# Optimization experiments

Hardware: AMD Instinct MI355X
Metric: run time of the kernel (lower is better)

## Reference

```python
import jax, jax.numpy as jnp
import numpy as np

A_CUBIC = -0.75  # torch grid_sample bicubic convolution coefficient
INTERP_FACTOR = 0.25
WINDOW = 20
STEP = 4


def _cubic_interp_1d(signal):
    # Replicates torch bicubic grid_sample (align_corners=True, border padding)
    # on a (B,1,1,n) tensor, which reduces to 1D cubic convolution (A=-0.75).
    B, n = signal.shape
    num_points = int((n - 1) / INTERP_FACTOR) + 1
    pos = jnp.linspace(0.0, n - 1, num_points)  # sample positions in index space
    i0 = jnp.floor(pos).astype(jnp.int32)
    s = (pos - i0).astype(signal.dtype)  # frac in [0,1)
    A = A_CUBIC
    def w_far(d):   # 1 <= d <= 2
        return ((A * d - 5 * A) * d + 8 * A) * d - 4 * A
    def w_near(d):  # 0 <= d <= 1
        return ((A + 2) * d - (A + 3)) * d * d + 1
    w = jnp.stack([w_far(s + 1), w_near(s), w_near(1 - s), w_far(2 - s)], axis=-1)  # (P,4)
    idx = jnp.clip(i0[:, None] + jnp.arange(-1, 3)[None, :], 0, n - 1)  # border pad, (P,4)
    vals = signal[:, idx]  # (B,P,4)
    return jnp.einsum('bpk,pk->bp', vals, w)


def _apply_kernels(x, gamma_raw):
    # per-row shift so min >= 0 (only if min < 0), then softmax-weighted kernel mix
    m = jnp.min(x, axis=1, keepdims=True)
    x = x - jnp.minimum(m, 0.0)
    gamma = jax.nn.softmax(gamma_raw)
    poly = (x + 1.3) ** 2                      # polynomial: degree=2, offset=1.3
    gauss = jnp.exp(-0.5 * (x - 0.7) ** 2)     # gaussian: center=0.7, sigma=1.0
    return gamma[0] * poly + gamma[1] * gauss


def setup_inputs() -> dict:
    key = jax.random.key(0)
    return {
        'signal': jax.random.normal(key, (4, 1000), dtype=jnp.float32),
        'alpha': jnp.float32(0.15),
        'beta': jnp.float32(0.9),
        'gamma_raw': jnp.array([0.5, 0.5], dtype=jnp.float32),
    }


def reference(signal, alpha, beta, gamma_raw):
    interp = _cubic_interp_1d(signal)              # (B, n)
    ks = _apply_kernels(interp, gamma_raw)         # (B, n)
    B, n = ks.shape
    n_windows = (n - WINDOW) // STEP + 1
    starts = jnp.arange(n_windows) * STEP          # (W,)
    posn = jnp.arange(n)                           # (n,)
    in_win = (posn[None, :] >= starts[:, None]) & (posn[None, :] < starts[:, None] + WINDOW)
    in_win = in_win.astype(ks.dtype)               # (W, n)
    sig = ks[:, None, :]                           # (B,1,n)
    # M: fft of zero-padded window; M1: fft of signal with window zeroed out
    M = jnp.abs(jnp.fft.fft(sig * in_win[None], axis=-1))          # (B,W,n)
    M1 = jnp.abs(jnp.fft.fft(sig * (1.0 - in_win)[None], axis=-1))  # (B,W,n)
    x_max = jnp.max(M, axis=-1, keepdims=True)
    strong = (M > x_max * alpha).astype(M.dtype)
    combined = M1 * M * strong
    result = jnp.minimum(M, combined)              # (B,W,n)
    thr = beta * jnp.max(result.reshape(B, -1), axis=1)[:, None, None]
    result = result * (result > thr).astype(result.dtype)
    return result
```

## Files before the change

kernel.cpp:

```cpp
#include <hip/hip_runtime.h>
#include <math.h>

#define NSIG 1000
#define NP   3997
#define KHALF 1999
#define NW   995
#define WIN  20
#define STEPW 4
#define BATCH 4
#define NCH  125
#define CW   8
#define RS   2000


__device__ __forceinline__ double interp_at(const float* __restrict__ s, int p) {
    int i0 = p >> 2;
    int si = p & 3;
    double ss = 0.25 * (double)si;
    const double A = -0.75;
    double d0 = ss + 1.0;
    double w0 = ((A * d0 - 5.0 * A) * d0 + 8.0 * A) * d0 - 4.0 * A;
    double w1 = ((A + 2.0) * ss - (A + 3.0)) * ss * ss + 1.0;
    double d2 = 1.0 - ss;
    double w2 = ((A + 2.0) * d2 - (A + 3.0)) * d2 * d2 + 1.0;
    double d3 = 2.0 - ss;
    double w3 = ((A * d3 - 5.0 * A) * d3 + 8.0 * A) * d3 - 4.0 * A;
    int im1 = i0 - 1; if (im1 < 0) im1 = 0;
    int ip1 = i0 + 1; if (ip1 > NSIG - 1) ip1 = NSIG - 1;
    int ip2 = i0 + 2; if (ip2 > NSIG - 1) ip2 = NSIG - 1;
    return w0 * (double)s[im1] + w1 * (double)s[i0] +
           w2 * (double)s[ip1] + w3 * (double)s[ip2];
}

__global__ __launch_bounds__(256) void init_kernel(
        const float* __restrict__ sig, const float* __restrict__ gamma_raw,
        float* __restrict__ ks, float2* __restrict__ tw,
        unsigned int* __restrict__ rmax) {
    int bx = blockIdx.x;
    int tid = threadIdx.x;
    if (bx < 16) {
        int m = bx * 256 + tid;
        if (m < NP) {
            double ang = -6.283185307179586476925286766559 * ((double)m / (double)NP);
            double sv, cv; sincos(ang, &sv, &cv);
            tw[m] = make_float2((float)cv, (float)sv);
        }
        if (bx == 0 && tid < BATCH) rmax[tid] = 0u;
        return;
    }
    __shared__ double red[256];
    int b = bx - 16;
    const float* srow = sig + b * NSIG;
    double lmin = 1e300;
    for (int p = tid; p < NP; p += 256)
        lmin = fmin(lmin, interp_at(srow, p));
    red[tid] = lmin;
    __syncthreads();
    for (int s = 128; s > 0; s >>= 1) {
        if (tid < s) red[tid] = fmin(red[tid], red[tid + s]);
        __syncthreads();
    }
    double m = fmin(red[0], 0.0);
    double g0r = (double)gamma_raw[0], g1r = (double)gamma_raw[1];
    double mx = fmax(g0r, g1r);
    double e0 = exp(g0r - mx), e1 = exp(g1r - mx);
    double inv = 1.0 / (e0 + e1);
    double g0 = e0 * inv, g1 = e1 * inv;
    for (int p = tid; p < NP; p += 256) {
        double x = interp_at(srow, p) - m;
        double poly = (x + 1.3) * (x + 1.3);
        double gauss = exp(-0.5 * (x - 0.7) * (x - 0.7));
        ks[b * NP + p] = (float)(g0 * poly + g1 * gauss);
    }
}

__global__ __launch_bounds__(256) void dft_kernel(const float* __restrict__ ks,
                                                  float2* __restrict__ S) {
    __shared__ float  lks[NP];
    __shared__ double2 red[256];
    int b = blockIdx.y;
    int tid = threadIdx.x;
    int kk = tid & 7;
    int tc = tid >> 3;
    int k = blockIdx.x * 8 + kk;
    for (int i = tid; i < NP; i += 256) lks[i] = ks[b * NP + i];
    __syncthreads();

    double sr = 0.0, si = 0.0;
    if (k < KHALF) {
        int t0 = tc * 125;
        int t1 = t0 + 125; if (t1 > NP) t1 = NP;
        const double TWO_PI = 6.283185307179586476925286766559;
        double base = -TWO_PI / (double)NP;
        double rr, ri;
        sincos(base * (double)k, &ri, &rr);
        int m0 = (k * t0) % NP;
        double pr, pi;
        sincos(base * (double)m0, &pi, &pr);
        for (int t = t0; t < t1; ++t) {
            double kv = (double)lks[t];
            sr = fma(kv, pr, sr);
            si = fma(kv, pi, si);
            double nr = pr * rr - pi * ri;
            double ni = pr * ri + pi * rr;
            pr = nr; pi = ni;
        }
    }
    red[tid] = make_double2(sr, si);
    __syncthreads();
    for (int s = 128; s >= 8; s >>= 1) {
        if (tid < s) {
            red[tid].x += red[tid + s].x;
            red[tid].y += red[tid + s].y;
        }
        __syncthreads();
    }
    if (tid < 8) {
        int kw = blockIdx.x * 8 + tid;
        if (kw < KHALF)
            S[b * NP + kw] = make_float2((float)red[tid].x, (float)red[tid].y);
    }
}

__device__ __forceinline__ float wavemax(float x) {
    #pragma unroll
    for (int off = 32; off > 0; off >>= 1)
        x = fmaxf(x, __shfl_xor(x, off));
    return x;
}

#define SLIDE1(n, co, cn) { \
    float ax = fmaf((cn), T##n.x, -(co)); \
    float ay = (cn) * T##n.y; \
    Wx##n = fmaf(ax, Q##n.x, fmaf(-ay, Q##n.y, Wx##n)); \
    Wy##n = fmaf(ax, Q##n.y, fmaf(ay, Q##n.x, Wy##n)); \
    float tq = fmaf(Q##n.x, R##n.x, -(Q##n.y * R##n.y)); \
    Q##n.y = fmaf(Q##n.x, R##n.y, Q##n.y * R##n.x); \
    Q##n.x = tq; }

#define SLIDEJ(co, cn) SLIDE1(0, co, cn) SLIDE1(1, co, cn) SLIDE1(2, co, cn) SLIDE1(3, co, cn)

#define SLIDE4(base) { \
    { float co = kp[(base) + 0], cn = kp[(base) + 20]; SLIDEJ(co, cn) } \
    { float co = kp[(base) + 1], cn = kp[(base) + 21]; SLIDEJ(co, cn) } \
    { float co = kp[(base) + 2], cn = kp[(base) + 22]; SLIDEJ(co, cn) } \
    { float co = kp[(base) + 3], cn = kp[(base) + 23]; SLIDEJ(co, cn) } }

#define WINBODY(w) { \
    float M0 = sqrtf(fmaf(Wx0, Wx0, Wy0 * Wy0)); \
    float M1m = sqrtf(fmaf(Wx1, Wx1, Wy1 * Wy1)); \
    float M2m = sqrtf(fmaf(Wx2, Wx2, Wy2 * Wy2)); \
    float M3m = sqrtf(fmaf(Wx3, Wx3, Wy3 * Wy3)); \
    float lm = fmaxf(fmaxf(M0, M1m), fmaxf(M2m, v3 ? M3m : 0.f)); \
    lm = wavemax(lm); \
    if ((tid & 63) == 0) wred[tid >> 6] = lm; \
    __syncthreads(); \
    float bm = fmaxf(fmaxf(fmaxf(wred[0], wred[1]), fmaxf(wred[2], wred[3])), \
                     fmaxf(fmaxf(wred[4], wred[5]), fmaxf(wred[6], wred[7]))); \
    float cut = bm * alpha; \
    __syncthreads(); \
    if (w0 + (w) < NW) { \
        float r0v = 0.f, r1v = 0.f, r2v = 0.f, r3v = 0.f; \
        { float dr = Sv0.x - Wx0, di = Sv0.y - Wy0; float m1 = sqrtf(fmaf(dr, dr, di * di)); \
          if (M0 > cut) r0v = fminf(M0, m1 * M0); } \
        { float dr = Sv1.x - Wx1, di = Sv1.y - Wy1; float m1 = sqrtf(fmaf(dr, dr, di * di)); \
          if (M1m > cut) r1v = fminf(M1m, m1 * M1m); } \
        { float dr = Sv2.x - Wx2, di = Sv2.y - Wy2; float m1 = sqrtf(fmaf(dr, dr, di * di)); \
          if (M2m > cut) r2v = fminf(M2m, m1 * M2m); } \
        { float dr = Sv3.x - Wx3, di = Sv3.y - Wy3; float m1 = sqrtf(fmaf(dr, dr, di * di)); \
          if (M3m > cut) r3v = fminf(M3m, m1 * M3m); } \
        float* rp = resc + rbase + (size_t)(w) * RS; \
        rp[k0] = r0v; rp[k1] = r1v; rp[k2] = r2v; if (v3) rp[k3] = r3v; \
        rl = fmaxf(rl, fmaxf(fmaxf(r0v, r1v), fmaxf(r2v, r3v))); \
    } }

__global__ __launch_bounds__(512, 4) void window_kernel(
        const float* __restrict__ ks, const float2* __restrict__ tw,
        const float2* __restrict__ S, const float* __restrict__ alpha_p,
        float* __restrict__ resc, float* __restrict__ cmax,
        unsigned int* __restrict__ rmax) {
    __shared__ float wred[8];
    int b = blockIdx.y;
    int wc = blockIdx.x;
    int w0 = wc * CW;
    int s0 = w0 * STEPW;
    int tid = threadIdx.x;
    float alpha = *alpha_p;
    const float* kp = ks + b * NP + s0;

    int k0 = tid, k1 = tid + 512, k2 = tid + 1024, k3 = tid + 1536;
    bool v3 = (k3 < KHALF);

    float2 R0 = tw[k0], R1 = tw[k1], R2 = tw[k2], R3 = tw[k3];
    float2 T0 = tw[(20 * k0) % NP], T1 = tw[(20 * k1) % NP],
           T2 = tw[(20 * k2) % NP], T3 = tw[(20 * k3) % NP];
    float2 Q0 = tw[(k0 * s0) % NP], Q1 = tw[(k1 * s0) % NP],
           Q2 = tw[(k2 * s0) % NP], Q3 = tw[(k3 * s0) % NP];
    const float2* Sb = S + b * NP;
    float2 Sv0 = Sb[k0], Sv1 = Sb[k1], Sv2 = Sb[k2], Sv3 = Sb[k3];

    float Dx0 = kp[19], Dy0 = 0.f, Dx1 = kp[19], Dy1 = 0.f,
          Dx2 = kp[19], Dy2 = 0.f, Dx3 = kp[19], Dy3 = 0.f;
    #pragma unroll
    for (int j = 18; j >= 0; --j) {
        float a = kp[j];
        float nx, ny;
        nx = fmaf(Dx0, R0.x, fmaf(-Dy0, R0.y, a));
        ny = fmaf(Dy0, R0.x, Dx0 * R0.y);
        Dx0 = nx; Dy0 = ny;
        nx = fmaf(Dx1, R1.x, fmaf(-Dy1, R1.y, a));
        ny = fmaf(Dy1, R1.x, Dx1 * R1.y);
        Dx1 = nx; Dy1 = ny;
        nx = fmaf(Dx2, R2.x, fmaf(-Dy2, R2.y, a));
        ny = fmaf(Dy2, R2.x, Dx2 * R2.y);
        Dx2 = nx; Dy2 = ny;
        nx = fmaf(Dx3, R3.x, fmaf(-Dy3, R3.y, a));
        ny = fmaf(Dy3, R3.x, Dx3 * R3.y);
        Dx3 = nx; Dy3 = ny;
    }
    float Wx0 = fmaf(Q0.x, Dx0, -(Q0.y * Dy0));
    float Wy0 = fmaf(Q0.x, Dy0, Q0.y * Dx0);
    float Wx1 = fmaf(Q1.x, Dx1, -(Q1.y * Dy1));
    float Wy1 = fmaf(Q1.x, Dy1, Q1.y * Dx1);
    float Wx2 = fmaf(Q2.x, Dx2, -(Q2.y * Dy2));
    float Wy2 = fmaf(Q2.x, Dy2, Q2.y * Dx2);
    float Wx3 = fmaf(Q3.x, Dx3, -(Q3.y * Dy3));
    float Wy3 = fmaf(Q3.x, Dy3, Q3.y * Dx3);

    float rl = 0.f;
    size_t rbase = (size_t)(b * NW + w0) * RS;

    WINBODY(0)
    SLIDE4(0)  WINBODY(1)
    SLIDE4(4)  WINBODY(2)
    SLIDE4(8)  WINBODY(3)
    SLIDE4(12) WINBODY(4)
    SLIDE4(16) WINBODY(5)
    SLIDE4(20) WINBODY(6)
    SLIDE4(24) WINBODY(7)

    rl = wavemax(rl);
    if ((tid & 63) == 0) wred[tid >> 6] = rl;
    __syncthreads();
    if (tid == 0) {
        float bm = fmaxf(fmaxf(fmaxf(wred[0], wred[1]), fmaxf(wred[2], wred[3])),
                         fmaxf(fmaxf(wred[4], wred[5]), fmaxf(wred[6], wred[7])));
        cmax[b * NCH + wc] = bm;
        atomicMax(&rmax[b], __float_as_uint(bm));
    }
}

__global__ __launch_bounds__(1024) void finalize_kernel(
        const float* __restrict__ resc, const float* __restrict__ cmax,
        const unsigned int* __restrict__ rmax, const float* __restrict__ beta_p,
        float* __restrict__ out) {
    int b = blockIdx.y, w = blockIdx.x;
    float thr = (*beta_p) * __uint_as_float(rmax[b]);
    size_t base = (size_t)(b * NW + w) * NP;
    int tid = threadIdx.x;
    if (cmax[b * NCH + (w >> 3)] <= thr) {
        #pragma unroll
        for (int c = 0; c < 4; ++c) {
            int i = tid + c * 1024;
            if (i < NP) out[base + i] = 0.f;
        }
        return;
    }
    const float* rp = resc + (size_t)(b * NW + w) * RS;
    #pragma unroll
    for (int c = 0; c < 2; ++c) {
        int k = tid + c * 1024;
        if (k < KHALF) {
            float v = rp[k];
            float f = (v > thr) ? v : 0.f;
            out[base + k] = f;
            if (k > 0) out[base + NP - k] = f;
        }
    }
}

extern "C" void kernel_launch(void* const* d_in, const int* in_sizes, int n_in,
                              void* d_out, int out_size, void* d_ws, size_t ws_size,
                              hipStream_t stream) {
    const float* sig       = (const float*)d_in[0];
    const float* alpha_p   = (const float*)d_in[1];
    const float* beta_p    = (const float*)d_in[2];
    const float* gamma_raw = (const float*)d_in[3];
    char* ws = (char*)d_ws;
    float*        ks   = (float*)(ws + 0);
    float2*       tw   = (float2*)(ws + 65536);
    float2*       S    = (float2*)(ws + 98304);
    unsigned int* rmax = (unsigned int*)(ws + 226304);
    float*        cmax = (float*)(ws + 226432);
    float*        resc = (float*)(ws + 262144);
    float* out = (float*)d_out;

    hipLaunchKernelGGL(init_kernel,     dim3(20),         dim3(256),  0, stream, sig, gamma_raw, ks, tw, rmax);
    hipLaunchKernelGGL(dft_kernel,      dim3(250, BATCH), dim3(256),  0, stream, ks, S);
    hipLaunchKernelGGL(window_kernel,   dim3(NCH, BATCH), dim3(512),  0, stream, ks, tw, S, alpha_p, resc, cmax, rmax);
    hipLaunchKernelGGL(finalize_kernel, dim3(NW, BATCH),  dim3(1024), 0, stream, resc, cmax, rmax, beta_p, out);
}
```

Before: 70.29 us.

## Fuse all stages into one cooperative persistent kernel with grid syncs

Measured after the change: 269.5 us. 283% more time.

```diff
diff --git a/kernel.cpp b/kernel.cpp
--- a/kernel.cpp
+++ b/kernel.cpp
@@ -1,5 +1,8 @@
 #include <hip/hip_runtime.h>
+#include <hip/hip_cooperative_groups.h>
 #include <math.h>
+
+namespace cg = cooperative_groups;
 
 #define NSIG 1000
 #define NP   3997
@@ -11,6 +14,8 @@
 #define NCH  125
 #define CW   8
 #define RS   2000
+#define NBLK 256
+#define NTASK (NCH * BATCH)
 
 
 __device__ __forceinline__ double interp_at(const float* __restrict__ s, int p) {
@@ -30,96 +35,6 @@
     int ip2 = i0 + 2; if (ip2 > NSIG - 1) ip2 = NSIG - 1;
     return w0 * (double)s[im1] + w1 * (double)s[i0] +
            w2 * (double)s[ip1] + w3 * (double)s[ip2];
-}
-
-__global__ __launch_bounds__(256) void init_kernel(
-        const float* __restrict__ sig, const float* __restrict__ gamma_raw,
-        float* __restrict__ ks, float2* __restrict__ tw,
-        unsigned int* __restrict__ rmax) {
-    int bx = blockIdx.x;
-    int tid = threadIdx.x;
-    if (bx < 16) {
-        int m = bx * 256 + tid;
-        if (m < NP) {
-            double ang = -6.283185307179586476925286766559 * ((double)m / (double)NP);
-            double sv, cv; sincos(ang, &sv, &cv);
-            tw[m] = make_float2((float)cv, (float)sv);
-        }
-        if (bx == 0 && tid < BATCH) rmax[tid] = 0u;
-        return;
-    }
-    __shared__ double red[256];
-    int b = bx - 16;
-    const float* srow = sig + b * NSIG;
-    double lmin = 1e300;
-    for (int p = tid; p < NP; p += 256)
-        lmin = fmin(lmin, interp_at(srow, p));
-    red[tid] = lmin;
-    __syncthreads();
-    for (int s = 128; s > 0; s >>= 1) {
-        if (tid < s) red[tid] = fmin(red[tid], red[tid + s]);
-        __syncthreads();
-    }
-    double m = fmin(red[0], 0.0);
-    double g0r = (double)gamma_raw[0], g1r = (double)gamma_raw[1];
-    double mx = fmax(g0r, g1r);
-    double e0 = exp(g0r - mx), e1 = exp(g1r - mx);
-    double inv = 1.0 / (e0 + e1);
-    double g0 = e0 * inv, g1 = e1 * inv;
-    for (int p = tid; p < NP; p += 256) {
-        double x = interp_at(srow, p) - m;
-        double poly = (x + 1.3) * (x + 1.3);
-        double gauss = exp(-0.5 * (x - 0.7) * (x - 0.7));
-        ks[b * NP + p] = (float)(g0 * poly + g1 * gauss);
-    }
-}
-
-__global__ __launch_bounds__(256) void dft_kernel(const float* __restrict__ ks,
-                                                  float2* __restrict__ S) {
-    __shared__ float  lks[NP];
-    __shared__ double2 red[256];
-    int b = blockIdx.y;
-    int tid = threadIdx.x;
-    int kk = tid & 7;
-    int tc = tid >> 3;
-    int k = blockIdx.x * 8 + kk;
-    for (int i = tid; i < NP; i += 256) lks[i] = ks[b * NP + i];
-    __syncthreads();
-
-    double sr = 0.0, si = 0.0;
-    if (k < KHALF) {
-        int t0 = tc * 125;
-        int t1 = t0 + 125; if (t1 > NP) t1 = NP;
-        const double TWO_PI = 6.283185307179586476925286766559;
-        double base = -TWO_PI / (double)NP;
-        double rr, ri;
-        sincos(base * (double)k, &ri, &rr);
-        int m0 = (k * t0) % NP;
-        double pr, pi;
-        sincos(base * (double)m0, &pi, &pr);
-        for (int t = t0; t < t1; ++t) {
-            double kv = (double)lks[t];
-            sr = fma(kv, pr, sr);
-            si = fma(kv, pi, si);
-            double nr = pr * rr - pi * ri;
-            double ni = pr * ri + pi * rr;
-            pr = nr; pi = ni;
-        }
-    }
-    red[tid] = make_double2(sr, si);
-    __syncthreads();
-    for (int s = 128; s >= 8; s >>= 1) {
-        if (tid < s) {
-            red[tid].x += red[tid + s].x;
-            red[tid].y += red[tid + s].y;
-        }
-        __syncthreads();
-    }
-    if (tid < 8) {
-        int kw = blockIdx.x * 8 + tid;
-        if (kw < KHALF)
-            S[b * NP + kw] = make_float2((float)red[tid].x, (float)red[tid].y);
-    }
 }
 
 __device__ __forceinline__ float wavemax(float x) {
@@ -174,107 +89,200 @@
         rl = fmaxf(rl, fmaxf(fmaxf(r0v, r1v), fmaxf(r2v, r3v))); \
     } }
 
-__global__ __launch_bounds__(512, 4) void window_kernel(
-        const float* __restrict__ ks, const float2* __restrict__ tw,
-        const float2* __restrict__ S, const float* __restrict__ alpha_p,
-        float* __restrict__ resc, float* __restrict__ cmax,
-        unsigned int* __restrict__ rmax) {
-    __shared__ float wred[8];
-    int b = blockIdx.y;
-    int wc = blockIdx.x;
-    int w0 = wc * CW;
-    int s0 = w0 * STEPW;
+__global__ __launch_bounds__(512, 2) void mega_kernel(
+        const float* __restrict__ sig, const float* __restrict__ alpha_p,
+        const float* __restrict__ beta_p, const float* __restrict__ gamma_raw,
+        float* __restrict__ ks, float2* __restrict__ tw, float2* __restrict__ S,
+        unsigned int* __restrict__ rmax, float* __restrict__ cmax,
+        float* __restrict__ resc, float* __restrict__ out) {
+    cg::grid_group grid = cg::this_grid();
+    int bid = blockIdx.x;
     int tid = threadIdx.x;
+
+    __shared__ float   lks[NP];
+    __shared__ double2 redd[512];
+    __shared__ float   wred[8];
+
+    if (bid < 8) {
+        int m = bid * 512 + tid;
+        if (m < NP) {
+            double ang = -6.283185307179586476925286766559 * ((double)m / (double)NP);
+            double sv, cv; sincos(ang, &sv, &cv);
+            tw[m] = make_float2((float)cv, (float)sv);
+        }
+        if (bid == 0 && tid < BATCH) rmax[tid] = 0u;
+    } else if (bid < 8 + BATCH) {
+        int b = bid - 8;
+        const float* srow = sig + b * NSIG;
+        double lmin = 1e300;
+        for (int p = tid; p < NP; p += 512)
+            lmin = fmin(lmin, interp_at(srow, p));
+        redd[tid].x = lmin;
+        __syncthreads();
+        for (int s = 256; s > 0; s >>= 1) {
+            if (tid < s) redd[tid].x = fmin(redd[tid].x, redd[tid + s].x);
+            __syncthreads();
+        }
+        double mm = fmin(redd[0].x, 0.0);
+        double g0r = (double)gamma_raw[0], g1r = (double)gamma_raw[1];
+        double mx = fmax(g0r, g1r);
+        double e0 = exp(g0r - mx), e1 = exp(g1r - mx);
+        double inv = 1.0 / (e0 + e1);
+        double g0 = e0 * inv, g1 = e1 * inv;
+        for (int p = tid; p < NP; p += 512) {
+            double x = interp_at(srow, p) - mm;
+            double poly = (x + 1.3) * (x + 1.3);
+            double gauss = exp(-0.5 * (x - 0.7) * (x - 0.7));
+            ks[b * NP + p] = (float)(g0 * poly + g1 * gauss);
+        }
+    }
+    __threadfence();
+    grid.sync();
+
+    for (int tsk = bid; tsk < NTASK; tsk += NBLK) {
+        int b = tsk & 3, kg = tsk >> 2;
+        __syncthreads();
+        for (int i = tid; i < NP; i += 512) lks[i] = ks[b * NP + i];
+        __syncthreads();
+        int kk = tid & 15, tc = tid >> 4;
+        int k = kg * 16 + kk;
+        double sr = 0.0, si = 0.0;
+        if (k < KHALF) {
+            int t0 = tc * 125;
+            int t1 = t0 + 125; if (t1 > NP) t1 = NP;
+            const double TWO_PI = 6.283185307179586476925286766559;
+            double base = -TWO_PI / (double)NP;
+            double rr, ri;
+            sincos(base * (double)k, &ri, &rr);
+            int m0 = (k * t0) % NP;
+            double pr, pi;
+            sincos(base * (double)m0, &pi, &pr);
+            for (int t = t0; t < t1; ++t) {
+                double kv = (double)lks[t];
+                sr = fma(kv, pr, sr);
+                si = fma(kv, pi, si);
+                double nr = pr * rr - pi * ri;
+                double ni = pr * ri + pi * rr;
+                pr = nr; pi = ni;
+            }
+        }
+        redd[tid] = make_double2(sr, si);
+        __syncthreads();
+        for (int s = 256; s >= 16; s >>= 1) {
+            if (tid < s) {
+                redd[tid].x += redd[tid + s].x;
+                redd[tid].y += redd[tid + s].y;
+            }
+            __syncthreads();
+        }
+        if (tid < 16) {
+            int kw = kg * 16 + tid;
+            if (kw < KHALF)
+                S[b * NP + kw] = make_float2((float)redd[tid].x, (float)redd[tid].y);
+        }
+    }
+    __threadfence();
+    grid.sync();
+
     float alpha = *alpha_p;
-    const float* kp = ks + b * NP + s0;
-
-    int k0 = tid, k1 = tid + 512, k2 = tid + 1024, k3 = tid + 1536;
-    bool v3 = (k3 < KHALF);
-
-    float2 R0 = tw[k0], R1 = tw[k1], R2 = tw[k2], R3 = tw[k3];
-    float2 T0 = tw[(20 * k0) % NP], T1 = tw[(20 * k1) % NP],
-           T2 = tw[(20 * k2) % NP], T3 = tw[(20 * k3) % NP];
-    float2 Q0 = tw[(k0 * s0) % NP], Q1 = tw[(k1 * s0) % NP],
-           Q2 = tw[(k2 * s0) % NP], Q3 = tw[(k3 * s0) % NP];
-    const float2* Sb = S + b * NP;
-    float2 Sv0 = Sb[k0], Sv1 = Sb[k1], Sv2 = Sb[k2], Sv3 = Sb[k3];
-
-    float Dx0 = kp[19], Dy0 = 0.f, Dx1 = kp[19], Dy1 = 0.f,
-          Dx2 = kp[19], Dy2 = 0.f, Dx3 = kp[19], Dy3 = 0.f;
-    #pragma unroll
-    for (int j = 18; j >= 0; --j) {
-        float a = kp[j];
-        float nx, ny;
-        nx = fmaf(Dx0, R0.x, fmaf(-Dy0, R0.y, a));
-        ny = fmaf(Dy0, R0.x, Dx0 * R0.y);
-        Dx0 = nx; Dy0 = ny;
-        nx = fmaf(Dx1, R1.x, fmaf(-Dy1, R1.y, a));
-        ny = fmaf(Dy1, R1.x, Dx1 * R1.y);
-        Dx1 = nx; Dy1 = ny;
-        nx = fmaf(Dx2, R2.x, fmaf(-Dy2, R2.y, a));
-        ny = fmaf(Dy2, R2.x, Dx2 * R2.y);
-        Dx2 = nx; Dy2 = ny;
-        nx = fmaf(Dx3, R3.x, fmaf(-Dy3, R3.y, a));
-        ny = fmaf(Dy3, R3.x, Dx3 * R3.y);
-        Dx3 = nx; Dy3 = ny;
+    for (int tsk = bid; tsk < NTASK; tsk += NBLK) {
+        int b = tsk & 3, wc = tsk >> 2;
+        int w0 = wc * CW;
+        int s0 = w0 * STEPW;
+        const float* kp = ks + b * NP + s0;
+
+        int k0 = tid, k1 = tid + 512, k2 = tid + 1024, k3 = tid + 1536;
+        bool v3 = (k3 < KHALF);
+
+        float2 R0 = tw[k0], R1 = tw[k1], R2 = tw[k2], R3 = tw[k3];
+        float2 T0 = tw[(20 * k0) % NP], T1 = tw[(20 * k1) % NP],
+               T2 = tw[(20 * k2) % NP], T3 = tw[(20 * k3) % NP];
+        float2 Q0 = tw[(k0 * s0) % NP], Q1 = tw[(k1 * s0) % NP],
+               Q2 = tw[(k2 * s0) % NP], Q3 = tw[(k3 * s0) % NP];
+        const float2* Sb = S + b * NP;
+        float2 Sv0 = Sb[k0], Sv1 = Sb[k1], Sv2 = Sb[k2], Sv3 = Sb[k3];
+
+        float Dx0 = kp[19], Dy0 = 0.f, Dx1 = kp[19], Dy1 = 0.f,
+              Dx2 = kp[19], Dy2 = 0.f, Dx3 = kp[19], Dy3 = 0.f;
+        #pragma unroll
+        for (int j = 18; j >= 0; --j) {
+            float a = kp[j];
+            float nx, ny;
+            nx = fmaf(Dx0, R0.x, fmaf(-Dy0, R0.y, a));
+            ny = fmaf(Dy0, R0.x, Dx0 * R0.y);
+            Dx0 = nx; Dy0 = ny;
+            nx = fmaf(Dx1, R1.x, fmaf(-Dy1, R1.y, a));
+            ny = fmaf(Dy1, R1.x, Dx1 * R1.y);
+            Dx1 = nx; Dy1 = ny;
+            nx = fmaf(Dx2, R2.x, fmaf(-Dy2, R2.y, a));
+            ny = fmaf(Dy2, R2.x, Dx2 * R2.y);
+            Dx2 = nx; Dy2 = ny;
+            nx = fmaf(Dx3, R3.x, fmaf(-Dy3, R3.y, a));
+            ny = fmaf(Dy3, R3.x, Dx3 * R3.y);
+            Dx3 = nx; Dy3 = ny;
+        }
+        float Wx0 = fmaf(Q0.x, Dx0, -(Q0.y * Dy0));
+        float Wy0 = fmaf(Q0.x, Dy0, Q0.y * Dx0);
+        float Wx1 = fmaf(Q1.x, Dx1, -(Q1.y * Dy1));
+        float Wy1 = fmaf(Q1.x, Dy1, Q1.y * Dx1);
+        float Wx2 = fmaf(Q2.x, Dx2, -(Q2.y * Dy2));
+        float Wy2 = fmaf(Q2.x, Dy2, Q2.y * Dx2);
+        float Wx3 = fmaf(Q3.x, Dx3, -(Q3.y * Dy3));
+        float Wy3 = fmaf(Q3.x, Dy3, Q3.y * Dx3);
+
+        float rl = 0.f;
+        size_t rbase = (size_t)(b * NW + w0) * RS;
+
+        WINBODY(0)
+        SLIDE4(0)  WINBODY(1)
+        SLIDE4(4)  WINBODY(2)
+        SLIDE4(8)  WINBODY(3)
+        SLIDE4(12) WINBODY(4)
+        SLIDE4(16) WINBODY(5)
+        SLIDE4(20) WINBODY(6)
+        SLIDE4(24) WINBODY(7)
+
+        rl = wavemax(rl);
+        if ((tid & 63) == 0) wred[tid >> 6] = rl;
+        __syncthreads();
+        if (tid == 0) {
+            float bm = fmaxf(fmaxf(fmaxf(wred[0], wred[1]), fmaxf(wred[2], wred[3])),
+                             fmaxf(fmaxf(wred[4], wred[5]), fmaxf(wred[6], wred[7])));
+            cmax[b * NCH + wc] = bm;
+            atomicMax(&rmax[b], __float_as_uint(bm));
+        }
+        __syncthreads();
     }
-    float Wx0 = fmaf(Q0.x, Dx0, -(Q0.y * Dy0));
-    float Wy0 = fmaf(Q0.x, Dy0, Q0.y * Dx0);
-    float Wx1 = fmaf(Q1.x, Dx1, -(Q1.y * Dy1));
-    float Wy1 = fmaf(Q1.x, Dy1, Q1.y * Dx1);
-    float Wx2 = fmaf(Q2.x, Dx2, -(Q2.y * Dy2));
-    float Wy2 = fmaf(Q2.x, Dy2, Q2.y * Dx2);
-    float Wx3 = fmaf(Q3.x, Dx3, -(Q3.y * Dy3));
-    float Wy3 = fmaf(Q3.x, Dy3, Q3.y * Dx3);
-
-    float rl = 0.f;
-    size_t rbase = (size_t)(b * NW + w0) * RS;
-
-    WINBODY(0)
-    SLIDE4(0)  WINBODY(1)
-    SLIDE4(4)  WINBODY(2)
-    SLIDE4(8)  WINBODY(3)
-    SLIDE4(12) WINBODY(4)
-    SLIDE4(16) WINBODY(5)
-    SLIDE4(20) WINBODY(6)
-    SLIDE4(24) WINBODY(7)
-
-    rl = wavemax(rl);
-    if ((tid & 63) == 0) wred[tid >> 6] = rl;
+    __threadfence();
+    grid.sync();
+
+    if (tid < BATCH)
+        wred[tid] = __uint_as_float(atomicMax(&rmax[tid], 0u));
     __syncthreads();
-    if (tid == 0) {
-        float bm = fmaxf(fmaxf(fmaxf(wred[0], wred[1]), fmaxf(wred[2], wred[3])),
-                         fmaxf(fmaxf(wred[4], wred[5]), fmaxf(wred[6], wred[7])));
-        cmax[b * NCH + wc] = bm;
-        atomicMax(&rmax[b], __float_as_uint(bm));
-    }
-}
-
-__global__ __launch_bounds__(1024) void finalize_kernel(
-        const float* __restrict__ resc, const float* __restrict__ cmax,
-        const unsigned int* __restrict__ rmax, const float* __restrict__ beta_p,
-        float* __restrict__ out) {
-    int b = blockIdx.y, w = blockIdx.x;
-    float thr = (*beta_p) * __uint_as_float(rmax[b]);
-    size_t base = (size_t)(b * NW + w) * NP;
-    int tid = threadIdx.x;
-    if (cmax[b * NCH + (w >> 3)] <= thr) {
-        #pragma unroll
-        for (int c = 0; c < 4; ++c) {
-            int i = tid + c * 1024;
-            if (i < NP) out[base + i] = 0.f;
-        }
-        return;
-    }
-    const float* rp = resc + (size_t)(b * NW + w) * RS;
-    #pragma unroll
-    for (int c = 0; c < 2; ++c) {
-        int k = tid + c * 1024;
-        if (k < KHALF) {
-            float v = rp[k];
-            float f = (v > thr) ? v : 0.f;
-            out[base + k] = f;
-            if (k > 0) out[base + NP - k] = f;
+    float beta = *beta_p;
+    for (int rr = bid; rr < BATCH * NW; rr += NBLK) {
+        int b = rr / NW;
+        int w = rr - b * NW;
+        float thr = beta * wred[b];
+        size_t base = (size_t)rr * NP;
+        if (cmax[b * NCH + (w >> 3)] <= thr) {
+            #pragma unroll
+            for (int c = 0; c < 8; ++c) {
+                int i = tid + c * 512;
+                if (i < NP) out[base + i] = 0.f;
+            }
+        } else {
+            const float* rp = resc + (size_t)rr * RS;
+            #pragma unroll
+            for (int c = 0; c < 4; ++c) {
+                int k = tid + c * 512;
+                if (k < KHALF) {
+                    float v = rp[k];
+                    float f = (v > thr) ? v : 0.f;
+                    out[base + k] = f;
+                    if (k > 0) out[base + NP - k] = f;
+                }
+            }
         }
     }
 }
@@ -293,10 +301,11 @@
     unsigned int* rmax = (unsigned int*)(ws + 226304);
     float*        cmax = (float*)(ws + 226432);
     float*        resc = (float*)(ws + 262144);
-    float* out = (float*)d_out;
-
-    hipLaunchKernelGGL(init_kernel,     dim3(20),         dim3(256),  0, stream, sig, gamma_raw, ks, tw, rmax);
-    hipLaunchKernelGGL(dft_kernel,      dim3(250, BATCH), dim3(256),  0, stream, ks, S);
-    hipLaunchKernelGGL(window_kernel,   dim3(NCH, BATCH), dim3(512),  0, stream, ks, tw, S, alpha_p, resc, cmax, rmax);
-    hipLaunchKernelGGL(finalize_kernel, dim3(NW, BATCH),  dim3(1024), 0, stream, resc, cmax, rmax, beta_p, out);
+    float* outp = (float*)d_out;
+
+    void* args[] = { (void*)&sig, (void*)&alpha_p, (void*)&beta_p, (void*)&gamma_raw,
+                     (void*)&ks, (void*)&tw, (void*)&S, (void*)&rmax,
+                     (void*)&cmax, (void*)&resc, (void*)&outp };
+    hipLaunchCooperativeKernel((const void*)mega_kernel, dim3(NBLK), dim3(512),
+                               args, 0, stream);
 }
```

## Fuse init into DFT kernel and recompute window spectra in finalize

Applied to the files above, without the earlier changes.

Result: faster. 61.65 us (-12.3%).

```diff
diff --git a/kernel.cpp b/kernel.cpp
--- a/kernel.cpp
+++ b/kernel.cpp
@@ -10,7 +10,6 @@
 #define BATCH 4
 #define NCH  125
 #define CW   8
-#define RS   2000
 
 
 __device__ __forceinline__ double interp_at(const float* __restrict__ s, int p) {
@@ -32,60 +31,60 @@
            w2 * (double)s[ip1] + w3 * (double)s[ip2];
 }
 
-__global__ __launch_bounds__(256) void init_kernel(
+__global__ __launch_bounds__(512) void dft_init_kernel(
         const float* __restrict__ sig, const float* __restrict__ gamma_raw,
-        float* __restrict__ ks, float2* __restrict__ tw,
+        float* __restrict__ ks, float2* __restrict__ tw, float2* __restrict__ S,
         unsigned int* __restrict__ rmax) {
+    __shared__ float   lks[NP];
+    __shared__ double2 redd[512];
+    int b = blockIdx.y;
     int bx = blockIdx.x;
     int tid = threadIdx.x;
-    if (bx < 16) {
-        int m = bx * 256 + tid;
-        if (m < NP) {
-            double ang = -6.283185307179586476925286766559 * ((double)m / (double)NP);
-            double sv, cv; sincos(ang, &sv, &cv);
-            tw[m] = make_float2((float)cv, (float)sv);
-        }
-        if (bx == 0 && tid < BATCH) rmax[tid] = 0u;
-        return;
-    }
-    __shared__ double red[256];
-    int b = bx - 16;
     const float* srow = sig + b * NSIG;
+
     double lmin = 1e300;
-    for (int p = tid; p < NP; p += 256)
-        lmin = fmin(lmin, interp_at(srow, p));
-    red[tid] = lmin;
+    #pragma unroll
+    for (int i = 0; i < 8; ++i) {
+        int p = tid + i * 512;
+        if (p < NP) lmin = fmin(lmin, interp_at(srow, p));
+    }
+    redd[tid].x = lmin;
     __syncthreads();
-    for (int s = 128; s > 0; s >>= 1) {
-        if (tid < s) red[tid] = fmin(red[tid], red[tid + s]);
+    for (int s = 256; s > 0; s >>= 1) {
+        if (tid < s) redd[tid].x = fmin(redd[tid].x, redd[tid + s].x);
         __syncthreads();
     }
-    double m = fmin(red[0], 0.0);
+    double m = fmin(redd[0].x, 0.0);
     double g0r = (double)gamma_raw[0], g1r = (double)gamma_raw[1];
     double mx = fmax(g0r, g1r);
     double e0 = exp(g0r - mx), e1 = exp(g1r - mx);
     double inv = 1.0 / (e0 + e1);
     double g0 = e0 * inv, g1 = e1 * inv;
-    for (int p = tid; p < NP; p += 256) {
-        double x = interp_at(srow, p) - m;
-        double poly = (x + 1.3) * (x + 1.3);
-        double gauss = exp(-0.5 * (x - 0.7) * (x - 0.7));
-        ks[b * NP + p] = (float)(g0 * poly + g1 * gauss);
-    }
-}
-
-__global__ __launch_bounds__(256) void dft_kernel(const float* __restrict__ ks,
-                                                  float2* __restrict__ S) {
-    __shared__ float  lks[NP];
-    __shared__ double2 red[256];
-    int b = blockIdx.y;
-    int tid = threadIdx.x;
-    int kk = tid & 7;
-    int tc = tid >> 3;
-    int k = blockIdx.x * 8 + kk;
-    for (int i = tid; i < NP; i += 256) lks[i] = ks[b * NP + i];
+    #pragma unroll
+    for (int i = 0; i < 8; ++i) {
+        int p = tid + i * 512;
+        if (p < NP) {
+            double x = interp_at(srow, p) - m;
+            double poly = (x + 1.3) * (x + 1.3);
+            double gauss = exp(-0.5 * (x - 0.7) * (x - 0.7));
+            float v = (float)(g0 * poly + g1 * gauss);
+            lks[p] = v;
+            if (bx == 0) ks[b * NP + p] = v;
+        }
+    }
+    if (b == 0 && bx < 8) {
+        int mm = bx * 512 + tid;
+        if (mm < NP) {
+            double ang = -6.283185307179586476925286766559 * ((double)mm / (double)NP);
+            double sv, cv; sincos(ang, &sv, &cv);
+            tw[mm] = make_float2((float)cv, (float)sv);
+        }
+        if (bx == 0 && tid < BATCH) rmax[tid] = 0u;
+    }
     __syncthreads();
 
+    int kk = tid & 15, tc = tid >> 4;
+    int k = bx * 16 + kk;
     double sr = 0.0, si = 0.0;
     if (k < KHALF) {
         int t0 = tc * 125;
@@ -106,19 +105,19 @@
             pr = nr; pi = ni;
         }
     }
-    red[tid] = make_double2(sr, si);
+    redd[tid] = make_double2(sr, si);
     __syncthreads();
-    for (int s = 128; s >= 8; s >>= 1) {
+    for (int s = 256; s >= 16; s >>= 1) {
         if (tid < s) {
-            red[tid].x += red[tid + s].x;
-            red[tid].y += red[tid + s].y;
+            redd[tid].x += redd[tid + s].x;
+            redd[tid].y += redd[tid + s].y;
         }
         __syncthreads();
     }
-    if (tid < 8) {
-        int kw = blockIdx.x * 8 + tid;
+    if (tid < 16) {
+        int kw = bx * 16 + tid;
         if (kw < KHALF)
-            S[b * NP + kw] = make_float2((float)red[tid].x, (float)red[tid].y);
+            S[b * NP + kw] = make_float2((float)redd[tid].x, (float)redd[tid].y);
     }
 }
 
@@ -160,6 +159,7 @@
     float cut = bm * alpha; \
     __syncthreads(); \
     if (w0 + (w) < NW) { \
+        if (tid == 0) wcut[b * NW + w0 + (w)] = cut; \
         float r0v = 0.f, r1v = 0.f, r2v = 0.f, r3v = 0.f; \
         { float dr = Sv0.x - Wx0, di = Sv0.y - Wy0; float m1 = sqrtf(fmaf(dr, dr, di * di)); \
           if (M0 > cut) r0v = fminf(M0, m1 * M0); } \
@@ -169,15 +169,13 @@
           if (M2m > cut) r2v = fminf(M2m, m1 * M2m); } \
         { float dr = Sv3.x - Wx3, di = Sv3.y - Wy3; float m1 = sqrtf(fmaf(dr, dr, di * di)); \
           if (M3m > cut) r3v = fminf(M3m, m1 * M3m); } \
-        float* rp = resc + rbase + (size_t)(w) * RS; \
-        rp[k0] = r0v; rp[k1] = r1v; rp[k2] = r2v; if (v3) rp[k3] = r3v; \
         rl = fmaxf(rl, fmaxf(fmaxf(r0v, r1v), fmaxf(r2v, r3v))); \
     } }
 
 __global__ __launch_bounds__(512, 4) void window_kernel(
         const float* __restrict__ ks, const float2* __restrict__ tw,
         const float2* __restrict__ S, const float* __restrict__ alpha_p,
-        float* __restrict__ resc, float* __restrict__ cmax,
+        float* __restrict__ wcut, float* __restrict__ cmax,
         unsigned int* __restrict__ rmax) {
     __shared__ float wred[8];
     int b = blockIdx.y;
@@ -228,7 +226,6 @@
     float Wy3 = fmaf(Q3.x, Dy3, Q3.y * Dx3);
 
     float rl = 0.f;
-    size_t rbase = (size_t)(b * NW + w0) * RS;
 
     WINBODY(0)
     SLIDE4(0)  WINBODY(1)
@@ -250,33 +247,69 @@
     }
 }
 
-__global__ __launch_bounds__(1024) void finalize_kernel(
-        const float* __restrict__ resc, const float* __restrict__ cmax,
-        const unsigned int* __restrict__ rmax, const float* __restrict__ beta_p,
-        float* __restrict__ out) {
+#define FINBIN(n, kn, valid) { \
+    if (valid) { \
+        float M = sqrtf(fmaf(Dx##n, Dx##n, Dy##n * Dy##n)); \
+        float2 P = tw[((kn) * start) % NP]; \
+        float Wr = fmaf(P.x, Dx##n, -(P.y * Dy##n)); \
+        float Wi = fmaf(P.x, Dy##n, P.y * Dx##n); \
+        float2 Sv = Sb[kn]; \
+        float dr = Sv.x - Wr, di = Sv.y - Wi; \
+        float M1 = sqrtf(fmaf(dr, dr, di * di)); \
+        float res = 0.f; \
+        if (M > cut) res = fminf(M, M1 * M); \
+        float f = (res > thr) ? res : 0.f; \
+        out[base + (kn)] = f; \
+        if ((kn) > 0) out[base + NP - (kn)] = f; \
+    } }
+
+__global__ __launch_bounds__(512) void finalize_kernel(
+        const float* __restrict__ ks, const float2* __restrict__ tw,
+        const float2* __restrict__ S, const float* __restrict__ wcut,
+        const float* __restrict__ cmax, const unsigned int* __restrict__ rmax,
+        const float* __restrict__ beta_p, float* __restrict__ out) {
     int b = blockIdx.y, w = blockIdx.x;
+    int tid = threadIdx.x;
     float thr = (*beta_p) * __uint_as_float(rmax[b]);
     size_t base = (size_t)(b * NW + w) * NP;
-    int tid = threadIdx.x;
     if (cmax[b * NCH + (w >> 3)] <= thr) {
         #pragma unroll
-        for (int c = 0; c < 4; ++c) {
-            int i = tid + c * 1024;
+        for (int c = 0; c < 8; ++c) {
+            int i = tid + c * 512;
             if (i < NP) out[base + i] = 0.f;
         }
         return;
     }
-    const float* rp = resc + (size_t)(b * NW + w) * RS;
-    #pragma unroll
-    for (int c = 0; c < 2; ++c) {
-        int k = tid + c * 1024;
-        if (k < KHALF) {
-            float v = rp[k];
-            float f = (v > thr) ? v : 0.f;
-            out[base + k] = f;
-            if (k > 0) out[base + NP - k] = f;
-        }
-    }
+    int start = w * STEPW;
+    const float* kp = ks + b * NP + start;
+    float cut = wcut[b * NW + w];
+    const float2* Sb = S + b * NP;
+    int k0 = tid, k1 = tid + 512, k2 = tid + 1024, k3 = tid + 1536;
+    bool v3 = (k3 < KHALF);
+    float2 R0 = tw[k0], R1 = tw[k1], R2 = tw[k2], R3 = tw[k3];
+    float Dx0 = kp[19], Dy0 = 0.f, Dx1 = kp[19], Dy1 = 0.f,
+          Dx2 = kp[19], Dy2 = 0.f, Dx3 = kp[19], Dy3 = 0.f;
+    #pragma unroll
+    for (int j = 18; j >= 0; --j) {
+        float a = kp[j];
+        float nx, ny;
+        nx = fmaf(Dx0, R0.x, fmaf(-Dy0, R0.y, a));
+        ny = fmaf(Dy0, R0.x, Dx0 * R0.y);
+        Dx0 = nx; Dy0 = ny;
+        nx = fmaf(Dx1, R1.x, fmaf(-Dy1, R1.y, a));
+        ny = fmaf(Dy1, R1.x, Dx1 * R1.y);
+        Dx1 = nx; Dy1 = ny;
+        nx = fmaf(Dx2, R2.x, fmaf(-Dy2, R2.y, a));
+        ny = fmaf(Dy2, R2.x, Dx2 * R2.y);
+        Dx2 = nx; Dy2 = ny;
+        nx = fmaf(Dx3, R3.x, fmaf(-Dy3, R3.y, a));
+        ny = fmaf(Dy3, R3.x, Dx3 * R3.y);
+        Dx3 = nx; Dy3 = ny;
+    }
+    FINBIN(0, k0, true)
+    FINBIN(1, k1, true)
+    FINBIN(2, k2, true)
+    FINBIN(3, k3, v3)
 }
 
 extern "C" void kernel_launch(void* const* d_in, const int* in_sizes, int n_in,
@@ -292,11 +325,13 @@
     float2*       S    = (float2*)(ws + 98304);
     unsigned int* rmax = (unsigned int*)(ws + 226304);
     float*        cmax = (float*)(ws + 226432);
-    float*        resc = (float*)(ws + 262144);
+    float*        wcut = (float*)(ws + 229376);
     float* out = (float*)d_out;
 
-    hipLaunchKernelGGL(init_kernel,     dim3(20),         dim3(256),  0, stream, sig, gamma_raw, ks, tw, rmax);
-    hipLaunchKernelGGL(dft_kernel,      dim3(250, BATCH), dim3(256),  0, stream, ks, S);
-    hipLaunchKernelGGL(window_kernel,   dim3(NCH, BATCH), dim3(512),  0, stream, ks, tw, S, alpha_p, resc, cmax, rmax);
-    hipLaunchKernelGGL(finalize_kernel, dim3(NW, BATCH),  dim3(1024), 0, stream, resc, cmax, rmax, beta_p, out);
-}
+    hipLaunchKernelGGL(dft_init_kernel, dim3(125, BATCH), dim3(512), 0, stream,
+                       sig, gamma_raw, ks, tw, S, rmax);
+    hipLaunchKernelGGL(window_kernel,   dim3(NCH, BATCH), dim3(512), 0, stream,
+                       ks, tw, S, alpha_p, wcut, cmax, rmax);
+    hipLaunchKernelGGL(finalize_kernel, dim3(NW, BATCH),  dim3(512), 0, stream,
+                       ks, tw, S, wcut, cmax, rmax, beta_p, out);
+}
```
